# Kernel tuning notes

Hardware: AMD Instinct MI355X
Metric: run time of the kernel (lower is better)

The kernel has to match this reference:

```python
import jax, jax.numpy as jnp
import numpy as np

NUM_NODES = 100000
NUM_EDGES = 3200000
N_PER = 400            # nodes per graph (equal-size graphs)
NUM_GRAPHS = 250
K = 100                # sort-pooling k
DIM = 32
IN_DIM = 128
TOTAL = 3 * DIM + 1    # 97 = concat channel count
GDIM = 128
OUT_DIM = 2
DENSE_DIM = (((K - 2) // 2 + 1) - 5 + 1) * 64  # 46*64 = 2944


def setup_inputs() -> dict:
    key = jax.random.key(0)
    ks = jax.random.split(key, 12)

    def lin(k, shape, fan_in):
        return jax.random.normal(k, shape, jnp.float32) / np.float32(np.sqrt(fan_in))

    return {
        "x": jax.random.normal(ks[0], (NUM_NODES, IN_DIM), jnp.float32),
        "edge_index": jax.random.randint(ks[1], (2, NUM_EDGES), 0, NUM_NODES, dtype=jnp.int32),
        "batch": jnp.arange(NUM_NODES, dtype=jnp.int32) // N_PER,
        "W1": lin(ks[2], (IN_DIM, DIM), IN_DIM), "b1": jnp.zeros((DIM,), jnp.float32),
        "W2": lin(ks[3], (DIM, DIM), DIM),       "b2": jnp.zeros((DIM,), jnp.float32),
        "W3": lin(ks[4], (DIM, DIM), DIM),       "b3": jnp.zeros((DIM,), jnp.float32),
        "W4": lin(ks[5], (DIM, 1), DIM),         "b4": jnp.zeros((1,), jnp.float32),
        "cw1": lin(ks[6], (128, 1, TOTAL), TOTAL),   "cb1": jnp.zeros((128,), jnp.float32),
        "cw2": lin(ks[7], (64, 128, 5), 128 * 5),    "cb2": jnp.zeros((64,), jnp.float32),
        "fw1": lin(ks[8], (GDIM, DENSE_DIM), DENSE_DIM), "fb1": jnp.zeros((GDIM,), jnp.float32),
        "fw3": lin(ks[9], (OUT_DIM, GDIM), GDIM),        "fb3": jnp.zeros((OUT_DIM,), jnp.float32),
    }


def _gcn(h_in, W, b, src, dst, coef, deg_inv):
    # GCNConv (improved=False): D^{-1/2}(A+I)D^{-1/2} (h W) + b
    h = h_in @ W
    agg = jax.ops.segment_sum(h[src] * coef, dst, num_segments=NUM_NODES)
    return agg + h * deg_inv[:, None] + b  # deg_inv = self-loop norm dis[i]^2


def reference(x, edge_index, batch, W1, b1, W2, b2, W3, b3, W4, b4,
              cw1, cb1, cw2, cb2, fw1, fb1, fw3, fb3):
    src, dst = edge_index[0], edge_index[1]
    deg = jax.ops.segment_sum(jnp.ones((NUM_EDGES,), x.dtype), dst, num_segments=NUM_NODES) + 1.0
    dis = jax.lax.rsqrt(deg)
    coef = (dis[src] * dis[dst])[:, None]
    deg_inv = 1.0 / deg

    x1 = jnp.tanh(_gcn(x,  W1, b1, src, dst, coef, deg_inv))
    x2 = jnp.tanh(_gcn(x1, W2, b2, src, dst, coef, deg_inv))
    x3 = jnp.tanh(_gcn(x2, W3, b3, src, dst, coef, deg_inv))
    x4 = jnp.tanh(_gcn(x2, W4, b4, src, dst, coef, deg_inv))  # NB: conv4 consumes x2 (as in source)
    xc = jnp.concatenate([x1, x2, x3, x4], axis=1)  # [N, 97]

    # global_sort_pool: per-graph descending sort by last channel, keep top K nodes
    order = jnp.lexsort((-xc[:, -1], batch))  # primary: graph id, secondary: -last channel
    xs = xc[order].reshape(NUM_GRAPHS, N_PER, TOTAL)[:, :K]  # [B, K, 97]

    # Conv1d(1, 128, kernel=stride=97) over flattened [B,1,K*97] == per-slot linear map
    c1 = jax.nn.relu(jnp.einsum('bkt,ct->bck', xs, cw1[:, 0, :]) + cb1[None, :, None])  # [B,128,K]
    p1 = c1.reshape(NUM_GRAPHS, 128, K // 2, 2).max(axis=-1)  # MaxPool1d(2,2) -> [B,128,50]
    c2 = jax.lax.conv_general_dilated(p1, cw2, (1,), 'VALID',
                                      dimension_numbers=('NCH', 'OIH', 'NCH'))
    c2 = jax.nn.relu(c2 + cb2[None, :, None])  # [B,64,46]

    flat = c2.reshape(NUM_GRAPHS, -1)            # [B, 2944]
    h = jax.nn.relu(flat @ fw1.T + fb1)          # fc1 + relu (dropout = identity in eval)
    logits = h @ fw3.T + fb3                     # fc3
    return jax.nn.log_softmax(logits, axis=-1)
```

## Files before the change

### kernel.cpp

```cpp
#include <hip/hip_runtime.h>
#include <hip/hip_bf16.h>

#define NNODES 100000
#define NEDGES 3200000
#define NPER   400
#define NGRAPH 250
#define KTOP   100
#define DIM    32
#define INDIM  128
#define TOTALC 97
#define BSHIFT 7
#define BNODES 128
#define NBUCK  782
#define NCHUNK 200
#define CHSZ   16000
#define BCAP   8192
#define BCCAP  8192

__device__ __forceinline__ float bf(unsigned short u) {
    return __uint_as_float(((unsigned)u) << 16);
}
__device__ __forceinline__ unsigned short f2bf(float f) {
    unsigned u = __float_as_uint(f);
    unsigned r = ((u >> 16) & 1u) + 0x7FFFu;
    return (unsigned short)((u + r) >> 16);
}

#define OW_W1   0
#define OW_B1   4096
#define OW_W2   4128
#define OW_B2   5152
#define OW_W3   5184
#define OW_B3   6208
#define OW_W4   6240
#define OW_B4   6272
#define OW_CW1  6280
#define OW_CB1  18696
#define OW_CW2  18824
#define OW_CB2  59784
#define OW_FW1  59848
#define OW_FB1  436680
#define OW_FW3  436808
#define OW_FB3  437064
#define OW_TOT  437072

struct Srcs { const void* p[16]; };

__global__ void k_setup(const unsigned int* __restrict__ xw, Srcs sr,
                        float* __restrict__ dst, float* __restrict__ fw1t,
                        float* __restrict__ w2t8, int* __restrict__ flag,
                        float* __restrict__ hb, float* __restrict__ x1b,
                        float* __restrict__ x2b, float* __restrict__ h4b,
                        int* __restrict__ gcur) {
    __shared__ int cs[256];
    int t = threadIdx.x;
    int c = 0;
    for (int i = t; i < 4096; i += 256) {
        unsigned e = (xw[i] >> 23) & 0xFFu;
        if (e >= 100u && e <= 150u) c++;
    }
    cs[t] = c;
    __syncthreads();
    for (int off = 128; off > 0; off >>= 1) {
        if (t < off) cs[t] += cs[t + off];
        __syncthreads();
    }
    int isb = (cs[0] < 2048) ? 1 : 0;
    if (blockIdx.x == 0) {
        if (t == 0) flag[0] = isb;
        if (t < 32) {
            hb[(size_t)NNODES * DIM + t]  = 0.f;
            x1b[(size_t)NNODES * DIM + t] = 0.f;
            x2b[(size_t)NNODES * DIM + t] = 0.f;
        }
        if (t == 32) h4b[NNODES] = 0.f;
        for (int i = t; i < NBUCK; i += 256) gcur[i] = i * BCAP;
    }
    long idx = (long)blockIdx.x * 256 + t;
    if (idx < OW_TOT) {
        const int st[16] = {OW_W1, OW_B1, OW_W2, OW_B2, OW_W3, OW_B3, OW_W4, OW_B4,
                            OW_CW1, OW_CB1, OW_CW2, OW_CB2, OW_FW1, OW_FB1, OW_FW3, OW_FB3};
        const int nn[16] = {4096, 32, 1024, 32, 1024, 32, 32, 1,
                            12416, 128, 40960, 64, 376832, 128, 256, 2};
        #pragma unroll
        for (int s = 0; s < 16; s++) {
            if (idx >= st[s] && idx < st[s] + nn[s]) {
                int l = (int)idx - st[s];
                dst[idx] = isb ? bf(((const unsigned short*)sr.p[s])[l])
                               : ((const float*)sr.p[s])[l];
            }
        }
    } else if (idx < OW_TOT + 376832) {
        int i2 = (int)(idx - OW_TOT);
        float v = isb ? bf(((const unsigned short*)sr.p[12])[i2])
                      : ((const float*)sr.p[12])[i2];
        int j = i2 / 2944, d = i2 - j * 2944;
        fw1t[d * 128 + j] = v;
    } else if (idx < OW_TOT + 376832 + 65536) {
        int k = (int)(idx - OW_TOT - 376832);
        int q = k & 7;
        int co = k >> 3;
        int cc = co >> 6, o = co & 63;
        float v = 0.f;
        if (q < 5) {
            int si = (o * 128 + cc) * 5 + q;
            v = isb ? bf(((const unsigned short*)sr.p[10])[si])
                    : ((const float*)sr.p[10])[si];
        }
        w2t8[k] = v;
    }
}

__global__ __launch_bounds__(1024) void
k_scatter(const int* __restrict__ ei, int* __restrict__ gcur,
          unsigned* __restrict__ staged) {
    __shared__ int h[NBUCK];
    __shared__ int cur[NBUCK];
    int c = blockIdx.x, t = threadIdx.x;
    for (int i = t; i < NBUCK; i += 1024) h[i] = 0;
    __syncthreads();
    int base = c * CHSZ;
    for (int e = base + t; e < base + CHSZ; e += 1024)
        atomicAdd(&h[ei[NEDGES + e] >> BSHIFT], 1);
    __syncthreads();
    for (int i = t; i < NBUCK; i += 1024) {
        int n = h[i];
        cur[i] = n ? atomicAdd(&gcur[i], n) : 0;
    }
    __syncthreads();
    for (int e = base + t; e < base + CHSZ; e += 1024) {
        int s = ei[e], d = ei[NEDGES + e];
        int b = d >> BSHIFT;
        int pos = atomicAdd(&cur[b], 1);
        staged[pos] = ((unsigned)(d & (BNODES - 1)) << 17) | (unsigned)s;
    }
}

__global__ __launch_bounds__(256) void
k_csr(const unsigned* __restrict__ staged, const int* __restrict__ gcur,
      int* __restrict__ degi, float* __restrict__ dis, float* __restrict__ rdis,
      int* __restrict__ csr_src, int* __restrict__ row_off) {
    __shared__ int cnt[BNODES];
    __shared__ int sc[BNODES];
    __shared__ int rofs[BNODES];
    int b = blockIdx.x, t = threadIdx.x;
    if (t < BNODES) cnt[t] = 0;
    __syncthreads();
    int s0 = b * BCAP;
    int s1 = gcur[b];
    for (int i = s0 + t; i < s1; i += 256)
        atomicAdd(&cnt[staged[i] >> 17], 1);
    __syncthreads();
    int n0 = b << BSHIFT;
    int nn = min(BNODES, NNODES - n0);
    int dg = (t < nn) ? cnt[t] : 0;
    if (t < nn) {
        degi[n0 + t] = dg;
        float d = (float)(dg + 1);
        dis[n0 + t]  = rsqrtf(d);
        rdis[n0 + t] = sqrtf(d);
    }
    int pd = (dg + 7) & ~7;
    if (t < BNODES) sc[t] = pd;
    __syncthreads();
    for (int o = 1; o < BNODES; o <<= 1) {
        int u = (t >= o && t < BNODES) ? sc[t - o] : 0;
        __syncthreads();
        if (t < BNODES) sc[t] += u;
        __syncthreads();
    }
    if (t < BNODES) rofs[t] = b * BCCAP + sc[t] - pd;
    if (t < nn) row_off[n0 + t] = rofs[t];
    if (t < BNODES) cnt[t] = 0;
    __syncthreads();
    for (int i = s0 + t; i < s1; i += 256) {
        unsigned rec = staged[i];
        int dl = rec >> 17, s = rec & 0x1FFFF;
        int r = atomicAdd(&cnt[dl], 1);
        csr_src[rofs[dl] + r] = s;
    }
    __syncthreads();
    if (t < nn) {
        int d = cnt[t], dp = (d + 7) & ~7;
        for (int s2 = d; s2 < dp; s2++) csr_src[rofs[t] + s2] = NNODES;
    }
}


__global__ void k_mm1(const void* __restrict__ xraw, const float* __restrict__ W1f,
                      const int* __restrict__ flag, const float* __restrict__ dis,
                      float* __restrict__ h) {
    __shared__ float w[INDIM * DIM];
    __shared__ float xsh[8 * INDIM];
    int t = threadIdx.x;
    for (int i = t; i < INDIM * DIM; i += 256) w[i] = W1f[i];
    if (flag[0]) {
        const unsigned int* xsrc = (const unsigned int*)((const unsigned short*)xraw
                                   + (size_t)blockIdx.x * 8 * INDIM);
        for (int i = t; i < 512; i += 256) {
            unsigned u = xsrc[i];
            xsh[2 * i]     = __uint_as_float(u << 16);
            xsh[2 * i + 1] = __uint_as_float(u & 0xFFFF0000u);
        }
    } else {
        const float4* xsrc = (const float4*)((const float*)xraw + (size_t)blockIdx.x * 8 * INDIM);
        float4* xdst = (float4*)xsh;
        for (int i = t; i < 256; i += 256) xdst[i] = xsrc[i];
    }
    __syncthreads();
    int ln = t >> 5, c = t & 31;
    const float* xr = xsh + ln * INDIM;
    float acc = 0.f;
    #pragma unroll 8
    for (int j = 0; j < INDIM; j++) acc += xr[j] * w[j * DIM + c];
    int node = blockIdx.x * 8 + ln;
    h[(size_t)node * DIM + c] = acc * dis[node];
}

__global__ __launch_bounds__(256, 8) void
k_gather(const float* __restrict__ xin, const float* __restrict__ h4s,
         const int* __restrict__ csr_src,
         const int* __restrict__ row_off, const int* __restrict__ degi,
         const float* __restrict__ dis,
         const float* __restrict__ Wm,
         const float* __restrict__ bias,
         const float* __restrict__ w4v,
         const float* __restrict__ b4,
         float* __restrict__ xout, float* __restrict__ x4out,
         float* __restrict__ h4out, int scaleOut) {
    __shared__ float wsh[DIM * DIM];
    __shared__ float w4sh[DIM];
    __shared__ float zsh[8 * DIM];
    __shared__ float osh[8 * DIM];
    int t = threadIdx.x;
    if (Wm)  for (int i = t; i < DIM * DIM; i += 256) wsh[i] = Wm[i];
    if (w4v && t < DIM) w4sh[t] = w4v[t];
    int node = blockIdx.x * 8 + (t >> 5);
    int lane = t & 31;
    int wg   = t >> 5;
    int start = row_off[node];
    int cnt   = degi[node];
    int iters = (cnt + 7) >> 3;
    const int4* ip = (const int4*)(csr_src + start);
    float acc0 = 0.f, acc1 = 0.f;
    if (iters > 0) {
        int4 iA = ip[0], iB = ip[1];
        for (int k = 1; k < iters; k++) {
            int4 nA = ip[2 * k], nB = ip[2 * k + 1];
            acc0 += xin[(size_t)iA.x * DIM + lane];
            acc1 += xin[(size_t)iA.y * DIM + lane];
            acc0 += xin[(size_t)iA.z * DIM + lane];
            acc1 += xin[(size_t)iA.w * DIM + lane];
            acc0 += xin[(size_t)iB.x * DIM + lane];
            acc1 += xin[(size_t)iB.y * DIM + lane];
            acc0 += xin[(size_t)iB.z * DIM + lane];
            acc1 += xin[(size_t)iB.w * DIM + lane];
            iA = nA; iB = nB;
        }
        acc0 += xin[(size_t)iA.x * DIM + lane];
        acc1 += xin[(size_t)iA.y * DIM + lane];
        acc0 += xin[(size_t)iA.z * DIM + lane];
        acc1 += xin[(size_t)iA.w * DIM + lane];
        acc0 += xin[(size_t)iB.x * DIM + lane];
        acc1 += xin[(size_t)iB.y * DIM + lane];
        acc0 += xin[(size_t)iB.z * DIM + lane];
        acc1 += xin[(size_t)iB.w * DIM + lane];
    }
    float disv = dis[node];
    float z = (acc0 + acc1 + xin[(size_t)node * DIM + lane]) * disv;
    if (!Wm) {
        float outv = tanhf(z + bias[lane]);
        xout[(size_t)node * DIM + lane] = outv * disv;
    } else {
        zsh[wg * DIM + lane] = z;
        __syncthreads();
        const float* zr = zsh + wg * DIM;
        float a = bias[lane];
        #pragma unroll
        for (int j = 0; j < DIM; j++) a += zr[j] * wsh[j * DIM + lane];
        float outv = tanhf(a);
        xout[(size_t)node * DIM + lane] = scaleOut ? outv * disv : outv;
        if (h4out) {
            osh[wg * DIM + lane] = outv;
            __syncthreads();
            if (lane == 0) {
                const float* xr = osh + wg * DIM;
                float a4 = 0.f;
                #pragma unroll
                for (int j = 0; j < DIM; j++) a4 += xr[j] * w4sh[j];
                h4out[node] = a4 * disv;
            }
        }
    }
    if (h4s) {
        int cntp = iters << 3;
        float a4 = 0.f;
        for (int ee = lane; ee < cntp; ee += 32)
            a4 += h4s[csr_src[start + ee]];
        for (int off = 16; off > 0; off >>= 1) a4 += __shfl_xor(a4, off, 32);
        if (lane == 0) x4out[node] = tanhf((a4 + h4s[node]) * disv + b4[0]);
    }
}

__global__ __launch_bounds__(1024) void
k_sortconv1(const float* __restrict__ x1, const float* __restrict__ x2,
            const float* __restrict__ x3, const float* __restrict__ x4,
            const float* __restrict__ rdis,
            const float* __restrict__ cw1f, const float* __restrict__ cb1f,
            float* __restrict__ p1g) {
    __shared__ unsigned long long keys[512];
    __shared__ __align__(16) float xs[32 * 100];
    __shared__ __align__(16) float ws[32 * 128];
    __shared__ int nsh[KTOP];
    __shared__ float rdl[KTOP];
    int g = blockIdx.x, t = threadIdx.x;
    for (int i = t; i < 512; i += 1024) {
        unsigned long long kk = 0xFFFFFFFFFFFFFFFFULL;
        if (i < NPER) {
            unsigned u = __float_as_uint(x4[g * NPER + i]);
            u = (u & 0x80000000u) ? ~u : (u | 0x80000000u);
            kk = ((unsigned long long)(~u) << 32) | (unsigned)i;
        }
        keys[i] = kk;
    }
    __syncthreads();
    for (int k = 2; k <= 512; k <<= 1)
        for (int j = k >> 1; j > 0; j >>= 1) {
            for (int i = t; i < 512; i += 1024) {
                int l = i ^ j;
                if (l > i) {
                    unsigned long long a = keys[i], b = keys[l];
                    bool asc = ((i & k) == 0);
                    if ((a > b) == asc) { keys[i] = b; keys[l] = a; }
                }
            }
            __syncthreads();
        }
    if (t < KTOP) {
        int nid = g * NPER + (int)(unsigned)(keys[t] & 0xFFFFFFFFu);
        nsh[t] = nid;
        rdl[t] = rdis[nid];
    }
    int ct = (t & 31) * 4;
    int kt = (t >> 5) * 4;
    bool act = (t < 800);
    float acc[4][4] = {};
    for (int ch = 0; ch < 3; ch++) {
        const float* arr = (ch == 0) ? x1 : (ch == 1) ? x2 : x3;
        __syncthreads();
        for (int i = t; i < 3200; i += 1024) {
            int q = i & 31, k = i >> 5;
            float v = arr[(size_t)nsh[k] * 32 + q];
            if (ch < 2) v *= rdl[k];
            xs[q * 100 + k] = v;
        }
        for (int i = t; i < 4096; i += 1024) {
            int c = i & 127, q = i >> 7;
            ws[q * 128 + c] = cw1f[c * TOTALC + ch * 32 + q];
        }
        __syncthreads();
        if (act) {
            for (int q = 0; q < 32; q++) {
                float4 wv = *(const float4*)&ws[q * 128 + ct];
                float4 xv = *(const float4*)&xs[q * 100 + kt];
                float xa[4] = { xv.x, xv.y, xv.z, xv.w };
                float wa[4] = { wv.x, wv.y, wv.z, wv.w };
                #pragma unroll
                for (int a = 0; a < 4; a++)
                    #pragma unroll
                    for (int b = 0; b < 4; b++)
                        acc[a][b] += xa[a] * wa[b];
            }
        }
    }
    if (act) {
        float wa[4];
        #pragma unroll
        for (int b = 0; b < 4; b++) wa[b] = cw1f[(ct + b) * TOTALC + 96];
        #pragma unroll
        for (int a = 0; a < 4; a++) {
            float xv = x4[nsh[kt + a]];
            #pragma unroll
            for (int b = 0; b < 4; b++) acc[a][b] += xv * wa[b];
        }
        int jbase = kt >> 1;
        #pragma unroll
        for (int b = 0; b < 4; b++) {
            float bias = cb1f[ct + b];
            float m0 = fmaxf(fmaxf(acc[0][b], acc[1][b]) + bias, 0.f);
            float m1 = fmaxf(fmaxf(acc[2][b], acc[3][b]) + bias, 0.f);
            p1g[((size_t)g * 128 + ct + b) * 50 + jbase]     = m0;
            p1g[((size_t)g * 128 + ct + b) * 50 + jbase + 1] = m1;
        }
    }
}

__global__ __launch_bounds__(512) void
k_conv2(const float* __restrict__ p1g, const float* __restrict__ w2t8,
        const float* __restrict__ cb2f, float* __restrict__ flatg) {
    __shared__ __align__(16) float p1s[128 * 52];
    __shared__ float fl[64 * 25];
    int bid = blockIdx.x;
    int g = bid >> 1, ph = bid & 1;
    int t = threadIdx.x;
    int p0 = ph ? 24 : 0;
    int np = ph ? 22 : 24;
    for (int i = t; i < 128 * 50; i += 512) {
        int c = i / 50, p = i % 50;
        p1s[c * 52 + p] = p1g[(size_t)g * 6400 + i];
    }
    for (int i = t; i < 128 * 2; i += 512) {
        int c = i >> 1;
        p1s[c * 52 + 50 + (i & 1)] = 0.f;
    }
    for (int i = t; i < 64 * 25; i += 512) fl[i] = 0.f;
    __syncthreads();
    {
        int o = t & 63;
        int c8 = t >> 6;
        float acc[24];
        #pragma unroll
        for (int p = 0; p < 24; p++) acc[p] = 0.f;
        int cbeg = c8 * 16;
        for (int c = cbeg; c < cbeg + 16; c++) {
            const float4* wb = (const float4*)(w2t8 + (((size_t)c * 64 + o) << 3));
            float4 wA = wb[0], wB = wb[1];
            float w0 = wA.x, w1 = wA.y, w2 = wA.z, w3 = wA.w, w4 = wB.x;
            float win[28];
            const float4* wsrc = (const float4*)&p1s[c * 52 + p0];
            #pragma unroll
            for (int v = 0; v < 7; v++) {
                float4 f = wsrc[v];
                win[4 * v] = f.x; win[4 * v + 1] = f.y; win[4 * v + 2] = f.z; win[4 * v + 3] = f.w;
            }
            #pragma unroll
            for (int p = 0; p < 24; p++)
                acc[p] += win[p] * w0 + win[p + 1] * w1 + win[p + 2] * w2
                        + win[p + 3] * w3 + win[p + 4] * w4;
        }
        for (int p = 0; p < np; p++) atomicAdd(&fl[o * 25 + p], acc[p]);
    }
    __syncthreads();
    for (int i = t; i < 64 * 24; i += 512) {
        int o = i / 24, p = i - o * 24;
        if (p < np)
            flatg[(size_t)g * 2944 + o * 46 + p0 + p] = fmaxf(fl[o * 25 + p] + cb2f[o], 0.f);
    }
}

__global__ __launch_bounds__(1024) void
k_fc1(const float* __restrict__ flatg, const float* __restrict__ fw1t,
      float* __restrict__ hpart) {
    __shared__ float fls[5 * 368];
    __shared__ float hp[8 * 5 * 128];
    int b = blockIdx.x;
    int gt = b >> 3, kt = b & 7;
    int t = threadIdx.x;
    int g0 = gt * 5;
    int d0 = kt * 368;
    for (int i = t; i < 5 * 368; i += 1024) {
        int g = i / 368, dd = i - g * 368;
        fls[i] = flatg[(size_t)(g0 + g) * 2944 + d0 + dd];
    }
    __syncthreads();
    int og = t & 127, s8 = t >> 7;
    int ds = s8 * 46;
    const float* wp = fw1t + (size_t)(d0 + ds) * 128 + og;
    const float* f0 = fls + ds;
    float a0 = 0.f, a1 = 0.f, a2 = 0.f, a3 = 0.f, a4 = 0.f;
    #pragma unroll 2
    for (int d = 0; d < 46; d++) {
        float w = wp[(size_t)d * 128];
        a0 += f0[d]            * w;
        a1 += f0[368 + d]      * w;
        a2 += f0[2 * 368 + d]  * w;
        a3 += f0[3 * 368 + d]  * w;
        a4 += f0[4 * 368 + d]  * w;
    }
    hp[(s8 * 5 + 0) * 128 + og] = a0;
    hp[(s8 * 5 + 1) * 128 + og] = a1;
    hp[(s8 * 5 + 2) * 128 + og] = a2;
    hp[(s8 * 5 + 3) * 128 + og] = a3;
    hp[(s8 * 5 + 4) * 128 + og] = a4;
    __syncthreads();
    if (t < 640) {
        int g = t >> 7, o2 = t & 127;
        float s = 0.f;
        #pragma unroll
        for (int s2 = 0; s2 < 8; s2++) s += hp[(s2 * 5 + g) * 128 + o2];
        hpart[((size_t)kt * NGRAPH + g0 + g) * 128 + o2] = s;
    }
}

__global__ void k_fc3(const float* __restrict__ hpart, const float* __restrict__ fb1f,
                      const float* __restrict__ fw3f, const float* __restrict__ fb3f,
                      const int* __restrict__ flag, void* __restrict__ outp) {
    __shared__ float hsh[128];
    int g = blockIdx.x, t = threadIdx.x;
    float s = fb1f[t];
    #pragma unroll
    for (int kt = 0; kt < 8; kt++) s += hpart[((size_t)kt * NGRAPH + g) * 128 + t];
    hsh[t] = fmaxf(s, 0.f);
    __syncthreads();
    if (t < 64) {
        float h0 = hsh[t], h1 = hsh[t + 64];
        float l0 = h0 * fw3f[t] + h1 * fw3f[t + 64];
        float l1 = h0 * fw3f[128 + t] + h1 * fw3f[192 + t];
        #pragma unroll
        for (int off = 32; off > 0; off >>= 1) {
            l0 += __shfl_down(l0, off, 64);
            l1 += __shfl_down(l1, off, 64);
        }
        if (t == 0) {
            l0 += fb3f[0]; l1 += fb3f[1];
            float m = fmaxf(l0, l1);
            float lse = m + logf(expf(l0 - m) + expf(l1 - m));
            if (flag[0]) {
                unsigned short* ob = (unsigned short*)outp;
                ob[g * 2 + 0] = f2bf(l0 - lse);
                ob[g * 2 + 1] = f2bf(l1 - lse);
            } else {
                float* of = (float*)outp;
                of[g * 2 + 0] = l0 - lse;
                of[g * 2 + 1] = l1 - lse;
            }
        }
    }
}


extern "C" void kernel_launch(void* const* d_in, const int* in_sizes, int n_in,
                              void* d_out, int out_size, void* d_ws, size_t ws_size,
                              hipStream_t stream) {
    const void* x  = d_in[0];
    const int* ei  = (const int*)d_in[1];

    char* p = (char*)d_ws;
    auto alloc = [&](size_t bytes) -> void* {
        void* r = (void*)p;
        p += (bytes + 255) & ~(size_t)255;
        return r;
    };
    int*      flag    = (int*)alloc(256);
    float*    wcv     = (float*)alloc((size_t)OW_TOT * 4);
    float*    fw1t    = (float*)alloc((size_t)376832 * 4);
    int*      gcur    = (int*)alloc(1024 * 4);
    int*      degi    = (int*)alloc((size_t)NNODES * 4);
    int*      row_off = (int*)alloc((size_t)NNODES * 4);
    float*    dis     = (float*)alloc((size_t)NNODES * 4);
    float*    rdis    = (float*)alloc((size_t)NNODES * 4);
    unsigned* staged  = (unsigned*)alloc((size_t)NBUCK * BCAP * 4);
    int*      csr_src = (int*)alloc((size_t)NBUCK * BCCAP * 4);
    float*    hbuf    = (float*)alloc(((size_t)NNODES * DIM + 256) * 4);
    float*    h4buf   = (float*)alloc(((size_t)NNODES + 256) * 4);
    float*    x1      = (float*)alloc(((size_t)NNODES * DIM + 256) * 4);
    float*    x2      = (float*)alloc(((size_t)NNODES * DIM + 256) * 4);
    float*    x3      = (float*)alloc((size_t)NNODES * DIM * 4);
    float*    x4      = (float*)alloc((size_t)NNODES * 4);
    float*    p1g     = (float*)alloc((size_t)NGRAPH * 128 * 50 * 4);
    float*    w2t     = (float*)alloc((size_t)64 * 128 * 8 * 4);
    float*    flatg   = (float*)alloc((size_t)NGRAPH * 2944 * 4);
    float*    hpart   = (float*)alloc((size_t)8 * NGRAPH * 128 * 4);
    (void)in_sizes; (void)n_in; (void)out_size; (void)ws_size;

    Srcs sr;
    for (int i = 0; i < 16; i++) sr.p[i] = d_in[3 + i];
    k_setup<<<3436, 256, 0, stream>>>((const unsigned int*)x, sr, wcv, fw1t, w2t, flag,
                                      hbuf, x1, x2, h4buf, gcur);

    k_scatter<<<NCHUNK, 1024, 0, stream>>>(ei, gcur, staged);
    k_csr    <<<NBUCK, 256, 0, stream>>>(staged, gcur, degi, dis, rdis, csr_src, row_off);

    k_mm1   <<<12500, 256, 0, stream>>>(x, wcv + OW_W1, flag, dis, hbuf);
    k_gather<<<12500, 256, 0, stream>>>(hbuf, nullptr, csr_src, row_off, degi, dis,
                                        nullptr, wcv + OW_B1, nullptr, nullptr,
                                        x1, nullptr, nullptr, 1);
    k_gather<<<12500, 256, 0, stream>>>(x1, nullptr, csr_src, row_off, degi, dis,
                                        wcv + OW_W2, wcv + OW_B2, wcv + OW_W4, nullptr,
                                        x2, nullptr, h4buf, 1);
    k_gather<<<12500, 256, 0, stream>>>(x2, h4buf, csr_src, row_off, degi, dis,
                                        wcv + OW_W3, wcv + OW_B3, nullptr, wcv + OW_B4,
                                        x3, x4, nullptr, 0);

    k_sortconv1<<<NGRAPH, 1024, 0, stream>>>(x1, x2, x3, x4, rdis,
                                             wcv + OW_CW1, wcv + OW_CB1, p1g);
    k_conv2    <<<2 * NGRAPH, 512, 0, stream>>>(p1g, w2t, wcv + OW_CB2, flatg);
    k_fc1      <<<400, 1024, 0, stream>>>(flatg, fw1t, hpart);
    k_fc3      <<<NGRAPH, 128, 0, stream>>>(hpart, wcv + OW_FB1, wcv + OW_FW3, wcv + OW_FB3,
                                            flag, d_out);
}
```

Baseline: 513.8 us.

## Split sort-conv1 kernel into two half-channel blocks per graph, drop gather launch bounds

The sort plus conv1 kernel now launches two 512-thread blocks per graph, each computing 64 of the 128 output channels. Each block redundantly sorts the graph's 400 keys, reusing the xs shared buffer for the keys, so there are more, smaller blocks to spread across CUs. The gather kernel also loses its launch_bounds(256,8) hint, which changes the compiler's register budget. The price is duplicated sort and row-gather work in each block pair.

```diff
diff --git a/kernel.cpp b/kernel.cpp
--- a/kernel.cpp
+++ b/kernel.cpp
@@ -217,17 +217,16 @@
     h[(size_t)node * DIM + c] = acc * dis[node];
 }
 
-__global__ __launch_bounds__(256, 8) void
-k_gather(const float* __restrict__ xin, const float* __restrict__ h4s,
-         const int* __restrict__ csr_src,
-         const int* __restrict__ row_off, const int* __restrict__ degi,
-         const float* __restrict__ dis,
-         const float* __restrict__ Wm,
-         const float* __restrict__ bias,
-         const float* __restrict__ w4v,
-         const float* __restrict__ b4,
-         float* __restrict__ xout, float* __restrict__ x4out,
-         float* __restrict__ h4out, int scaleOut) {
+__global__ void k_gather(const float* __restrict__ xin, const float* __restrict__ h4s,
+                         const int* __restrict__ csr_src,
+                         const int* __restrict__ row_off, const int* __restrict__ degi,
+                         const float* __restrict__ dis,
+                         const float* __restrict__ Wm,
+                         const float* __restrict__ bias,
+                         const float* __restrict__ w4v,
+                         const float* __restrict__ b4,
+                         float* __restrict__ xout, float* __restrict__ x4out,
+                         float* __restrict__ h4out, int scaleOut) {
     __shared__ float wsh[DIM * DIM];
     __shared__ float w4sh[DIM];
     __shared__ float zsh[8 * DIM];
@@ -302,37 +301,37 @@
     }
 }
 
-__global__ __launch_bounds__(1024) void
-k_sortconv1(const float* __restrict__ x1, const float* __restrict__ x2,
-            const float* __restrict__ x3, const float* __restrict__ x4,
-            const float* __restrict__ rdis,
-            const float* __restrict__ cw1f, const float* __restrict__ cb1f,
-            float* __restrict__ p1g) {
-    __shared__ unsigned long long keys[512];
+__global__ __launch_bounds__(512) void
+k_sconv1(const float* __restrict__ x1, const float* __restrict__ x2,
+         const float* __restrict__ x3, const float* __restrict__ x4,
+         const float* __restrict__ rdis,
+         const float* __restrict__ cw1f, const float* __restrict__ cb1f,
+         float* __restrict__ p1g) {
     __shared__ __align__(16) float xs[32 * 100];
-    __shared__ __align__(16) float ws[32 * 128];
+    __shared__ __align__(16) float ws[32 * 64];
     __shared__ int nsh[KTOP];
     __shared__ float rdl[KTOP];
-    int g = blockIdx.x, t = threadIdx.x;
-    for (int i = t; i < 512; i += 1024) {
+    int bid = blockIdx.x;
+    int g = bid >> 1, half = bid & 1;
+    int t = threadIdx.x;
+    unsigned long long* keys = (unsigned long long*)xs;
+    {
         unsigned long long kk = 0xFFFFFFFFFFFFFFFFULL;
-        if (i < NPER) {
-            unsigned u = __float_as_uint(x4[g * NPER + i]);
+        if (t < NPER) {
+            unsigned u = __float_as_uint(x4[g * NPER + t]);
             u = (u & 0x80000000u) ? ~u : (u | 0x80000000u);
-            kk = ((unsigned long long)(~u) << 32) | (unsigned)i;
-        }
-        keys[i] = kk;
+            kk = ((unsigned long long)(~u) << 32) | (unsigned)t;
+        }
+        keys[t] = kk;
     }
     __syncthreads();
     for (int k = 2; k <= 512; k <<= 1)
         for (int j = k >> 1; j > 0; j >>= 1) {
-            for (int i = t; i < 512; i += 1024) {
-                int l = i ^ j;
-                if (l > i) {
-                    unsigned long long a = keys[i], b = keys[l];
-                    bool asc = ((i & k) == 0);
-                    if ((a > b) == asc) { keys[i] = b; keys[l] = a; }
-                }
+            int l = t ^ j;
+            if (l > t) {
+                unsigned long long a = keys[t], b = keys[l];
+                bool asc = ((t & k) == 0);
+                if ((a > b) == asc) { keys[t] = b; keys[l] = a; }
             }
             __syncthreads();
         }
@@ -341,27 +340,28 @@
         nsh[t] = nid;
         rdl[t] = rdis[nid];
     }
-    int ct = (t & 31) * 4;
-    int kt = (t >> 5) * 4;
-    bool act = (t < 800);
+    int ct = (t & 15) * 4;
+    int kt = (t >> 4) * 4;
+    bool act = (t < 400);
+    int cbase = half * 64;
     float acc[4][4] = {};
     for (int ch = 0; ch < 3; ch++) {
         const float* arr = (ch == 0) ? x1 : (ch == 1) ? x2 : x3;
         __syncthreads();
-        for (int i = t; i < 3200; i += 1024) {
+        for (int i = t; i < 3200; i += 512) {
             int q = i & 31, k = i >> 5;
             float v = arr[(size_t)nsh[k] * 32 + q];
             if (ch < 2) v *= rdl[k];
             xs[q * 100 + k] = v;
         }
-        for (int i = t; i < 4096; i += 1024) {
-            int c = i & 127, q = i >> 7;
-            ws[q * 128 + c] = cw1f[c * TOTALC + ch * 32 + q];
+        for (int i = t; i < 2048; i += 512) {
+            int c = i & 63, q = i >> 6;
+            ws[q * 64 + c] = cw1f[(cbase + c) * TOTALC + ch * 32 + q];
         }
         __syncthreads();
         if (act) {
             for (int q = 0; q < 32; q++) {
-                float4 wv = *(const float4*)&ws[q * 128 + ct];
+                float4 wv = *(const float4*)&ws[q * 64 + ct];
                 float4 xv = *(const float4*)&xs[q * 100 + kt];
                 float xa[4] = { xv.x, xv.y, xv.z, xv.w };
                 float wa[4] = { wv.x, wv.y, wv.z, wv.w };
@@ -376,7 +376,7 @@
     if (act) {
         float wa[4];
         #pragma unroll
-        for (int b = 0; b < 4; b++) wa[b] = cw1f[(ct + b) * TOTALC + 96];
+        for (int b = 0; b < 4; b++) wa[b] = cw1f[(cbase + ct + b) * TOTALC + 96];
         #pragma unroll
         for (int a = 0; a < 4; a++) {
             float xv = x4[nsh[kt + a]];
@@ -386,11 +386,11 @@
         int jbase = kt >> 1;
         #pragma unroll
         for (int b = 0; b < 4; b++) {
-            float bias = cb1f[ct + b];
+            float bias = cb1f[cbase + ct + b];
             float m0 = fmaxf(fmaxf(acc[0][b], acc[1][b]) + bias, 0.f);
             float m1 = fmaxf(fmaxf(acc[2][b], acc[3][b]) + bias, 0.f);
-            p1g[((size_t)g * 128 + ct + b) * 50 + jbase]     = m0;
-            p1g[((size_t)g * 128 + ct + b) * 50 + jbase + 1] = m1;
+            p1g[((size_t)g * 128 + cbase + ct + b) * 50 + jbase]     = m0;
+            p1g[((size_t)g * 128 + cbase + ct + b) * 50 + jbase + 1] = m1;
         }
     }
 }
@@ -582,10 +582,10 @@
                                         wcv + OW_W3, wcv + OW_B3, nullptr, wcv + OW_B4,
                                         x3, x4, nullptr, 0);
 
-    k_sortconv1<<<NGRAPH, 1024, 0, stream>>>(x1, x2, x3, x4, rdis,
+    k_sconv1<<<2 * NGRAPH, 512, 0, stream>>>(x1, x2, x3, x4, rdis,
                                              wcv + OW_CW1, wcv + OW_CB1, p1g);
-    k_conv2    <<<2 * NGRAPH, 512, 0, stream>>>(p1g, w2t, wcv + OW_CB2, flatg);
-    k_fc1      <<<400, 1024, 0, stream>>>(flatg, fw1t, hpart);
-    k_fc3      <<<NGRAPH, 128, 0, stream>>>(hpart, wcv + OW_FB1, wcv + OW_FW3, wcv + OW_FB3,
-                                            flag, d_out);
-}
+    k_conv2 <<<2 * NGRAPH, 512, 0, stream>>>(p1g, w2t, wcv + OW_CB2, flatg);
+    k_fc1   <<<400, 1024, 0, stream>>>(flatg, fw1t, hpart);
+    k_fc3   <<<NGRAPH, 128, 0, stream>>>(hpart, wcv + OW_FB1, wcv + OW_FW3, wcv + OW_FB3,
+                                         flag, d_out);
+}
```

Result: no change. 512.8 us (-0.2%).
